# Kernel optimization log

Measured on AMD Instinct MI355X. Metric: run time of the kernel, lower is better.

## Reference

```python
import jax, jax.numpy as jnp
import numpy as np

EPS = 1e-8      # torch cosine_similarity eps
MARGIN = 0.3    # clamp margin for negative pairs


def setup_inputs() -> dict:
    key = jax.random.key(0)
    k1, k2 = jax.random.split(key)
    N, D = 8192, 256
    hidden = jax.random.normal(k1, (N, D), dtype=jnp.float32)
    labels = jax.random.randint(k2, (N,), 0, 16, dtype=jnp.int64)
    return {"hidden": hidden, "labels": labels}


def reference(hidden, labels):
    N = hidden.shape[0]
    # torch cosine_similarity: x.y / (max(||x||,eps) * max(||y||,eps))
    norms = jnp.maximum(jnp.linalg.norm(hidden, axis=1, keepdims=True), EPS)
    xn = hidden / norms                         # [N, D]
    sim = xn @ xn.T                             # [N, N] Gram of cosine sims
    same = labels[:, None] == labels[None, :]   # [N, N] label equality
    per_pair = jnp.where(same, 1.0 - sim, jnp.maximum(sim - MARGIN, 0.0))
    upper = jnp.triu(jnp.ones((N, N), dtype=bool), k=1)  # i < j pairs only
    count = N * (N - 1) // 2
    loss = jnp.sum(jnp.where(upper, per_pair, 0.0)) / max(count, 1)
    return loss
```

## Files before the change

### kernel.cpp

```cpp
#include <hip/hip_runtime.h>
#include <hip/hip_bf16.h>
#include <hip/hip_fp8.h>

typedef float f32x16 __attribute__((ext_vector_type(16)));

constexpr int NROW = 8192;
constexpr int DCOL = 256;
constexpr int BM = 128;
constexpr int BKB = 128;
constexpr int NKT = DCOL / BKB;
constexpr int NT = NROW / BM;
constexpr int NTILES = NT * (NT + 1) / 2;
constexpr float MARGIN = 0.3f;

__device__ inline void gload16(const unsigned char* g, unsigned char* l) {
    __builtin_amdgcn_global_load_lds(
        (const __attribute__((address_space(1))) void*)g,
        (__attribute__((address_space(3))) void*)l, 16, 0, 0);
}

__global__ __launch_bounds__(256) void normalize_kernel(const float* __restrict__ hidden,
                                                        unsigned char* __restrict__ xn) {
    int wid = threadIdx.x >> 6, lane = threadIdx.x & 63;
    int row = (blockIdx.x << 2) + wid;
    const float4* src = reinterpret_cast<const float4*>(hidden + (size_t)row * DCOL);
    float4 v = src[lane];
    float ss = v.x * v.x + v.y * v.y + v.z * v.z + v.w * v.w;
    #pragma unroll
    for (int off = 32; off; off >>= 1) ss += __shfl_down(ss, off);
    ss = __shfl(ss, 0);
    float inv = 1.0f / fmaxf(sqrtf(ss), 1e-8f);
    __hip_fp8_e4m3 q0(v.x * inv), q1(v.y * inv), q2(v.z * inv), q3(v.w * inv);
    uchar4 o;
    o.x = *reinterpret_cast<unsigned char*>(&q0);
    o.y = *reinterpret_cast<unsigned char*>(&q1);
    o.z = *reinterpret_cast<unsigned char*>(&q2);
    o.w = *reinterpret_cast<unsigned char*>(&q3);
    reinterpret_cast<uchar4*>(xn + (size_t)row * DCOL)[lane] = o;
}

__global__ __launch_bounds__(256) void pairloss_kernel(const unsigned char* __restrict__ xn,
                                                       const int* __restrict__ labels,
                                                       float* __restrict__ partials) {
    __shared__ unsigned char As[2][BM * BKB];
    __shared__ unsigned char Bs[2][BM * BKB];
    __shared__ int lblA[BM], lblB[BM];
    __shared__ float wsum[4];

    int bid = (int)(blockIdx.x & 7) * (NTILES / 8) + (int)(blockIdx.x >> 3);
    int bi = 0, rem = bid;
    while (rem >= NT - bi) { rem -= NT - bi; ++bi; }
    int bj = bi + rem;

    int tid = threadIdx.x;
    int wid = tid >> 6, lane = tid & 63;
    int wr = wid >> 1, wc = wid & 1;
    int brow = bi * BM, bcol = bj * BM;

    if (tid < BM) lblA[tid] = labels[brow + tid];
    else          lblB[tid - BM] = labels[bcol + tid - BM];

    f32x16 acc[2][2] = {};

    int srow = lane >> 3;
    int schunk = (lane & 7) ^ srow;
    const unsigned char* gA0 = xn + (size_t)brow * DCOL;
    const unsigned char* gB0 = xn + (size_t)bcol * DCOL;
    int lo = lane & 31, hi = lane >> 5;

    auto stage = [&](int t, int b) {
        #pragma unroll
        for (int q = 0; q < 4; ++q) {
            int rg = (wid * 4 + q) * 8;
            int goff = (rg + srow) * DCOL + t * BKB + schunk * 16;
            gload16(gA0 + goff, &As[b][rg * BKB]);
            gload16(gB0 + goff, &Bs[b][rg * BKB]);
        }
    };
    auto compute = [&](int b) {
        #pragma unroll
        for (int kk = 0; kk < 8; ++kk) {
            long af[2], bfr[2];
            #pragma unroll
            for (int m = 0; m < 2; ++m) {
                int r = wr * 64 + m * 32 + lo;
                af[m] = *reinterpret_cast<const long*>(
                    &As[b][r * BKB + ((kk ^ (r & 7)) << 4) + hi * 8]);
            }
            #pragma unroll
            for (int n = 0; n < 2; ++n) {
                int r = wc * 64 + n * 32 + lo;
                bfr[n] = *reinterpret_cast<const long*>(
                    &Bs[b][r * BKB + ((kk ^ (r & 7)) << 4) + hi * 8]);
            }
            __builtin_amdgcn_s_setprio(1);
            #pragma unroll
            for (int m = 0; m < 2; ++m)
                #pragma unroll
                for (int n = 0; n < 2; ++n)
                    acc[m][n] = __builtin_amdgcn_mfma_f32_32x32x16_fp8_fp8(af[m], bfr[n], acc[m][n], 0, 0, 0);
            __builtin_amdgcn_s_setprio(0);
        }
    };

    stage(0, 0);
    for (int t = 0; t < NKT; ++t) {
        int c = t & 1;
        asm volatile("s_waitcnt vmcnt(0)" ::: "memory");
        __builtin_amdgcn_s_barrier();
        if (t + 1 < NKT) stage(t + 1, c ^ 1);
        compute(c);
    }

    float local = 0.0f;
    #pragma unroll
    for (int m = 0; m < 2; ++m) {
        #pragma unroll
        for (int n = 0; n < 2; ++n) {
            #pragma unroll
            for (int g = 0; g < 16; ++g) {
                int crow = (g & 3) + 8 * (g >> 2) + 4 * hi;
                int il = wr * 64 + m * 32 + crow;
                int jl = wc * 64 + n * 32 + lo;
                int gi = brow + il, gj = bcol + jl;
                float sim = acc[m][n][g];
                float v = (lblA[il] == lblB[jl]) ? (1.0f - sim) : fmaxf(sim - MARGIN, 0.0f);
                local += (gi < gj) ? v : 0.0f;
            }
        }
    }
    #pragma unroll
    for (int off = 32; off; off >>= 1) local += __shfl_down(local, off);
    if (lane == 0) wsum[wid] = local;
    __syncthreads();
    if (tid == 0) partials[bid] = wsum[0] + wsum[1] + wsum[2] + wsum[3];
}

__global__ __launch_bounds__(512) void finalize_kernel(const float* __restrict__ partials,
                                                       float* __restrict__ out) {
    __shared__ float wsum[8];
    int tid = threadIdx.x, wid = tid >> 6, lane = tid & 63;
    float s = 0.0f;
    for (int i = tid; i < NTILES; i += 512) s += partials[i];
    #pragma unroll
    for (int off = 32; off; off >>= 1) s += __shfl_down(s, off);
    if (lane == 0) wsum[wid] = s;
    __syncthreads();
    if (tid == 0) {
        float total = 0.0f;
        #pragma unroll
        for (int w = 0; w < 8; ++w) total += wsum[w];
        out[0] = total * (1.0f / 33550336.0f);
    }
}

extern "C" void kernel_launch(void* const* d_in, const int* in_sizes, int n_in,
                              void* d_out, int out_size, void* d_ws, size_t ws_size,
                              hipStream_t stream) {
    const float* hidden = (const float*)d_in[0];
    const int* labels = (const int*)d_in[1];
    float* out = (float*)d_out;

    unsigned char* xn = (unsigned char*)d_ws;
    float* partials = (float*)((char*)d_ws + (size_t)NROW * DCOL);

    normalize_kernel<<<NROW / 4, 256, 0, stream>>>(hidden, xn);
    pairloss_kernel<<<NTILES, 256, 0, stream>>>(xn, labels, partials);
    finalize_kernel<<<1, 512, 0, stream>>>(partials, out);
}
```

Measured before the change: 40.82 us.

## Make pairloss blocks persistent over four tiles with cross-tile prefetch

Each block now handles four consecutive upper-triangular tiles. It prefetches the next tile's first K-slice while computing the current tile's second slice, so global loads overlap MFMA work across tile boundaries. Labels are read straight from global memory instead of being staged in shared memory, and per-wave partials are written directly, which removes the end-of-tile __syncthreads. The grid shrinks by a factor of four, which lowers launch parallelism and can make load balance worse. The blockIdx swizzle that spread tiles across XCDs is also dropped.

```diff
diff --git a/kernel.cpp b/kernel.cpp
--- a/kernel.cpp
+++ b/kernel.cpp
@@ -8,9 +8,10 @@
 constexpr int DCOL = 256;
 constexpr int BM = 128;
 constexpr int BKB = 128;
-constexpr int NKT = DCOL / BKB;
 constexpr int NT = NROW / BM;
 constexpr int NTILES = NT * (NT + 1) / 2;
+constexpr int TPB = 4;
+constexpr int NBLK = NTILES / TPB;
 constexpr float MARGIN = 0.3f;
 
 __device__ inline void gload16(const unsigned char* g, unsigned char* l) {
@@ -44,96 +45,108 @@
                                                        float* __restrict__ partials) {
     __shared__ unsigned char As[2][BM * BKB];
     __shared__ unsigned char Bs[2][BM * BKB];
-    __shared__ int lblA[BM], lblB[BM];
-    __shared__ float wsum[4];
-
-    int bid = (int)(blockIdx.x & 7) * (NTILES / 8) + (int)(blockIdx.x >> 3);
-    int bi = 0, rem = bid;
-    while (rem >= NT - bi) { rem -= NT - bi; ++bi; }
-    int bj = bi + rem;
 
     int tid = threadIdx.x;
     int wid = tid >> 6, lane = tid & 63;
     int wr = wid >> 1, wc = wid & 1;
-    int brow = bi * BM, bcol = bj * BM;
-
-    if (tid < BM) lblA[tid] = labels[brow + tid];
-    else          lblB[tid - BM] = labels[bcol + tid - BM];
-
-    f32x16 acc[2][2] = {};
-
+    int lo = lane & 31, hi = lane >> 5;
     int srow = lane >> 3;
     int schunk = (lane & 7) ^ srow;
-    const unsigned char* gA0 = xn + (size_t)brow * DCOL;
-    const unsigned char* gB0 = xn + (size_t)bcol * DCOL;
-    int lo = lane & 31, hi = lane >> 5;
 
-    auto stage = [&](int t, int b) {
+    int bi = 0, rem = (int)blockIdx.x * TPB;
+    while (rem >= NT - bi) { rem -= NT - bi; ++bi; }
+    int curBrow = bi * BM, curBcol = (bi + rem) * BM;
+
+    auto stage = [&](int brow, int bcol, int s, int b) {
+        const unsigned char* gA0 = xn + (size_t)brow * DCOL;
+        const unsigned char* gB0 = xn + (size_t)bcol * DCOL;
         #pragma unroll
         for (int q = 0; q < 4; ++q) {
             int rg = (wid * 4 + q) * 8;
-            int goff = (rg + srow) * DCOL + t * BKB + schunk * 16;
+            int goff = (rg + srow) * DCOL + s * BKB + schunk * 16;
             gload16(gA0 + goff, &As[b][rg * BKB]);
             gload16(gB0 + goff, &Bs[b][rg * BKB]);
         }
     };
-    auto compute = [&](int b) {
-        #pragma unroll
-        for (int kk = 0; kk < 8; ++kk) {
-            long af[2], bfr[2];
+
+    stage(curBrow, curBcol, 0, 0);
+
+    for (int k = 0; k < TPB; ++k) {
+        int nrem = rem + 1, nbi = bi;
+        if (nrem >= NT - nbi) { nrem = 0; ++nbi; }
+        int nxtBrow = nbi * BM, nxtBcol = (nbi + nrem) * BM;
+
+        f32x16 acc[2][2] = {};
+
+        auto compute = [&](int b) {
+            #pragma unroll
+            for (int kk = 0; kk < 8; ++kk) {
+                long af[2], bfr[2];
+                #pragma unroll
+                for (int m = 0; m < 2; ++m) {
+                    int r = wr * 64 + m * 32 + lo;
+                    af[m] = *reinterpret_cast<const long*>(
+                        &As[b][r * BKB + ((kk ^ (r & 7)) << 4) + hi * 8]);
+                }
+                #pragma unroll
+                for (int n = 0; n < 2; ++n) {
+                    int r = wc * 64 + n * 32 + lo;
+                    bfr[n] = *reinterpret_cast<const long*>(
+                        &Bs[b][r * BKB + ((kk ^ (r & 7)) << 4) + hi * 8]);
+                }
+                __builtin_amdgcn_s_setprio(1);
+                #pragma unroll
+                for (int m = 0; m < 2; ++m)
+                    #pragma unroll
+                    for (int n = 0; n < 2; ++n)
+                        acc[m][n] = __builtin_amdgcn_mfma_f32_32x32x16_fp8_fp8(af[m], bfr[n], acc[m][n], 0, 0, 0);
+                __builtin_amdgcn_s_setprio(0);
+            }
+        };
+
+        asm volatile("s_waitcnt vmcnt(0)" ::: "memory");
+        __builtin_amdgcn_s_barrier();
+        stage(curBrow, curBcol, 1, 1);
+        compute(0);
+
+        asm volatile("s_waitcnt vmcnt(0)" ::: "memory");
+        __builtin_amdgcn_s_barrier();
+        if (k + 1 < TPB) stage(nxtBrow, nxtBcol, 0, 0);
+        compute(1);
+
+        {
+            bool diag = (curBrow == curBcol);
+            int lb0 = labels[curBcol + wc * 64 + lo];
+            int lb1 = labels[curBcol + wc * 64 + 32 + lo];
+            float local = 0.0f;
             #pragma unroll
             for (int m = 0; m < 2; ++m) {
-                int r = wr * 64 + m * 32 + lo;
-                af[m] = *reinterpret_cast<const long*>(
-                    &As[b][r * BKB + ((kk ^ (r & 7)) << 4) + hi * 8]);
+                #pragma unroll
+                for (int g = 0; g < 16; ++g) {
+                    int crow = (g & 3) + 8 * (g >> 2) + 4 * hi;
+                    int il = wr * 64 + m * 32 + crow;
+                    int la = labels[curBrow + il];
+                    {
+                        float sim = acc[m][0][g];
+                        float v = (la == lb0) ? (1.0f - sim) : fmaxf(sim - MARGIN, 0.0f);
+                        if (diag) v = (il < wc * 64 + lo) ? v : 0.0f;
+                        local += v;
+                    }
+                    {
+                        float sim = acc[m][1][g];
+                        float v = (la == lb1) ? (1.0f - sim) : fmaxf(sim - MARGIN, 0.0f);
+                        if (diag) v = (il < wc * 64 + 32 + lo) ? v : 0.0f;
+                        local += v;
+                    }
+                }
             }
             #pragma unroll
-            for (int n = 0; n < 2; ++n) {
-                int r = wc * 64 + n * 32 + lo;
-                bfr[n] = *reinterpret_cast<const long*>(
-                    &Bs[b][r * BKB + ((kk ^ (r & 7)) << 4) + hi * 8]);
-            }
-            __builtin_amdgcn_s_setprio(1);
-            #pragma unroll
-            for (int m = 0; m < 2; ++m)
-                #pragma unroll
-                for (int n = 0; n < 2; ++n)
-                    acc[m][n] = __builtin_amdgcn_mfma_f32_32x32x16_fp8_fp8(af[m], bfr[n], acc[m][n], 0, 0, 0);
-            __builtin_amdgcn_s_setprio(0);
+            for (int off = 32; off; off >>= 1) local += __shfl_down(local, off);
+            if (lane == 0) partials[((int)blockIdx.x * TPB + k) * 4 + wid] = local;
         }
-    };
 
-    stage(0, 0);
-    for (int t = 0; t < NKT; ++t) {
-        int c = t & 1;
-        asm volatile("s_waitcnt vmcnt(0)" ::: "memory");
-        __builtin_amdgcn_s_barrier();
-        if (t + 1 < NKT) stage(t + 1, c ^ 1);
-        compute(c);
+        bi = nbi; rem = nrem; curBrow = nxtBrow; curBcol = nxtBcol;
     }
-
-    float local = 0.0f;
-    #pragma unroll
-    for (int m = 0; m < 2; ++m) {
-        #pragma unroll
-        for (int n = 0; n < 2; ++n) {
-            #pragma unroll
-            for (int g = 0; g < 16; ++g) {
-                int crow = (g & 3) + 8 * (g >> 2) + 4 * hi;
-                int il = wr * 64 + m * 32 + crow;
-                int jl = wc * 64 + n * 32 + lo;
-                int gi = brow + il, gj = bcol + jl;
-                float sim = acc[m][n][g];
-                float v = (lblA[il] == lblB[jl]) ? (1.0f - sim) : fmaxf(sim - MARGIN, 0.0f);
-                local += (gi < gj) ? v : 0.0f;
-            }
-        }
-    }
-    #pragma unroll
-    for (int off = 32; off; off >>= 1) local += __shfl_down(local, off);
-    if (lane == 0) wsum[wid] = local;
-    __syncthreads();
-    if (tid == 0) partials[bid] = wsum[0] + wsum[1] + wsum[2] + wsum[3];
 }
 
 __global__ __launch_bounds__(512) void finalize_kernel(const float* __restrict__ partials,
@@ -141,7 +154,7 @@
     __shared__ float wsum[8];
     int tid = threadIdx.x, wid = tid >> 6, lane = tid & 63;
     float s = 0.0f;
-    for (int i = tid; i < NTILES; i += 512) s += partials[i];
+    for (int i = tid; i < NTILES * 4; i += 512) s += partials[i];
     #pragma unroll
     for (int off = 32; off; off >>= 1) s += __shfl_down(s, off);
     if (lane == 0) wsum[wid] = s;
@@ -165,6 +178,6 @@
     float* partials = (float*)((char*)d_ws + (size_t)NROW * DCOL);
 
     normalize_kernel<<<NROW / 4, 256, 0, stream>>>(hidden, xn);
-    pairloss_kernel<<<NTILES, 256, 0, stream>>>(xn, labels, partials);
+    pairloss_kernel<<<NBLK, 256, 0, stream>>>(xn, labels, partials);
     finalize_kernel<<<1, 512, 0, stream>>>(partials, out);
 }
```

Measured after the change: 54.18 us. +32.7%, slower.
